# Optimization experiments

Measured on AMD Instinct MI355X. Metric: run time of the kernel, lower is better.

The kernel has to match this reference:

```python
import jax, jax.numpy as jnp
import numpy as np
import math

NUM_HEADS = 12
HEAD_DIM = 64
DEGREE = 3
POLY_DIM = HEAD_DIM * (DEGREE + 1)  # 256
MEM_HID = 512
HIDDEN = 768


def setup_inputs() -> dict:
    key = jax.random.key(0)
    ks = jax.random.split(key, 6)
    B, S = 4, 2048
    hidden_states = jax.random.normal(ks[0], (B, S, HIDDEN), dtype=jnp.float32)
    # q projection weight stored (in, out) so y = x @ Wq
    Wq = jax.random.normal(ks[1], (HIDDEN, HIDDEN), dtype=jnp.float32) / np.sqrt(HIDDEN)
    # polynomial coefficients initialized to 1/i!
    coeffs = jnp.array([1.0 / math.factorial(i) for i in range(DEGREE + 1)], dtype=jnp.float32)
    # deep memory MLP: Linear(poly_dim->mem_hid) + ReLU + Linear(mem_hid->poly_dim)
    W1 = jax.random.normal(ks[2], (POLY_DIM, MEM_HID), dtype=jnp.float32) / np.sqrt(POLY_DIM)
    b1 = jnp.zeros((MEM_HID,), dtype=jnp.float32)
    W2 = jax.random.normal(ks[3], (MEM_HID, POLY_DIM), dtype=jnp.float32) / np.sqrt(MEM_HID)
    b2 = jnp.zeros((POLY_DIM,), dtype=jnp.float32)
    return {"hidden_states": hidden_states, "Wq": Wq, "coeffs": coeffs,
            "W1": W1, "b1": b1, "W2": W2, "b2": b2}


def _poly_map(x, coeffs):
    # x: [..., head_dim] -> [..., head_dim*(degree+1)]
    xs = jnp.clip(x, -10.0, 10.0)
    feats = [coeffs[0] * jnp.ones_like(x)]
    for i in range(1, DEGREE + 1):
        feats.append(jnp.clip(coeffs[i] * xs ** i, -1e6, 1e6))
    return jnp.concatenate(feats, axis=-1)


def reference(hidden_states, Wq, coeffs, W1, b1, W2, b2):
    B, S, H = hidden_states.shape
    # q projection -> [B, S, nh, hd]
    q = (hidden_states @ Wq).reshape(B, S, NUM_HEADS, HEAD_DIM)
    # polynomial feature expansion -> [B, S, nh, poly_dim]
    poly_q = _poly_map(q, coeffs)
    flat = poly_q.reshape(-1, POLY_DIM)  # [B*S*nh, poly_dim]
    # deep memory MLP (test-time memory read)
    h = jax.nn.relu(flat @ W1 + b1)
    mem = h @ W2 + b2  # [B*S*nh, poly_dim]
    # slice first head_dim dims, fold heads back into hidden
    out = mem[:, :HEAD_DIM].reshape(B, S, NUM_HEADS * HEAD_DIM)
    return out
```

## Files before the change

kernel.cpp:

```cpp
#include <hip/hip_runtime.h>


typedef unsigned short u16;
typedef __attribute__((ext_vector_type(8))) short short8;
typedef __attribute__((ext_vector_type(4))) float f32x4;
typedef __attribute__((ext_vector_type(4))) u16 u16x4;

__device__ __forceinline__ u16 f2bf(float f) {
    unsigned u = __builtin_bit_cast(unsigned, f);
    u += 0x7FFFu + ((u >> 16) & 1u);
    return (u16)(u >> 16);
}

__device__ __forceinline__ unsigned cvtpk_bf16(float lo, float hi) {
    unsigned r;
    asm("v_cvt_pk_bf16_f32 %0, %1, %2" : "=v"(r) : "v"(lo), "v"(hi));
    return r;
}

__device__ __forceinline__ void gl2lds16(const void* g, void* l) {
    __builtin_amdgcn_global_load_lds(
        (const __attribute__((address_space(1))) unsigned int*)g,
        (__attribute__((address_space(3))) unsigned int*)l, 16, 0, 0);
}

#define WAIT_VM_LGKM_BAR(N) \
    asm volatile("s_waitcnt vmcnt(" #N ") lgkmcnt(0)\n\ts_barrier" ::: "memory")
#define WAIT_LGKM_BAR() \
    asm volatile("s_waitcnt lgkmcnt(0)\n\ts_barrier" ::: "memory")


__global__ __launch_bounds__(256)
void prep(const float* __restrict__ X, u16* __restrict__ Xb,
          const float* __restrict__ Wq, u16* __restrict__ Wqb,
          const float* __restrict__ W1, u16* __restrict__ W1b,
          const float* __restrict__ W2, u16* __restrict__ W2b,
          const float* __restrict__ b1, const float* __restrict__ coeffs,
          float* __restrict__ b1e)
{
    __shared__ float t[32][33];
    const int b = blockIdx.x, tid = threadIdx.x;

    if (b < 6144) {
        const int i = b * 256 + tid;
        float4 v = reinterpret_cast<const float4*>(X)[i];
        u16x4 o = {f2bf(v.x), f2bf(v.y), f2bf(v.z), f2bf(v.w)};
        reinterpret_cast<u16x4*>(Xb)[i] = o;
    } else if (b < 6880) {
        const float* in; u16* out; int R, Cin, bx, by;
        int lb = b - 6144;
        if (lb < 576)      { in = Wq; out = Wqb; R = 768; Cin = 768; bx = lb % 24; by = lb / 24; }
        else if (lb < 704) { lb -= 576; in = W1; out = W1b; R = 256; Cin = 512; bx = lb % 16; by = lb / 16; }
        else               { lb -= 704; in = W2; out = W2b; R = 512; Cin = 256; bx = lb % 2;  by = lb / 2; }
        const int c0 = bx * 32, r0 = by * 32;
        const int tx = tid & 31, ty = tid >> 5;
        #pragma unroll
        for (int j = 0; j < 32; j += 8)
            t[ty + j][tx] = in[(size_t)(r0 + ty + j) * Cin + c0 + tx];
        __syncthreads();
        #pragma unroll
        for (int j = 0; j < 32; j += 8)
            out[(size_t)(c0 + ty + j) * R + r0 + tx] = f2bf(t[tx][ty + j]);
    } else {
        const int n = (b - 6880) * 256 + tid;
        float s = 0.f;
        #pragma unroll 8
        for (int k = 0; k < 64; ++k) s += W1[k * 512 + n];
        b1e[n] = b1[n] + coeffs[0] * s;
    }
}


__global__ __launch_bounds__(256, 3)
void gemm1_poly(const u16* __restrict__ Xb, const u16* __restrict__ Wqb,
                const float* __restrict__ coeffs, u16* __restrict__ P)
{
    __shared__ u16 lds[128 * 200];

    const int tid = threadIdx.x;
    const int w = tid >> 6, lane = tid & 63;
    const int lrow = lane >> 2, lslot = lane & 3;
    const int m16 = lane & 15, quad = lane >> 4;
    const int w0 = w & 1, w1 = w >> 1;
    const int tok0 = blockIdx.x * 64;
    const int bn = blockIdx.y * 128;
    const int h0 = blockIdx.y * 2;

    const float c1 = coeffs[1], c2 = coeffs[2], c3 = coeffs[3];

    f32x4 acc[4][2];
    #pragma unroll
    for (int i = 0; i < 4; ++i)
        #pragma unroll
        for (int j = 0; j < 2; ++j)
            acc[i][j] = (f32x4){0.f, 0.f, 0.f, 0.f};

    auto stage = [&](int slot, int g) {
        const int k0 = g * 32;
        u16* Xs = lds + slot * 6144;
        u16* Ws = Xs + 2048;
        {
            const int row = w * 16 + lrow;
            const int cc = lslot ^ ((row >> 2) & 3);
            gl2lds16(Xb + (size_t)(tok0 + row) * 768 + k0 + cc * 8, &Xs[row * 32 + lslot * 8]);
        }
        #pragma unroll
        for (int i = 0; i < 2; ++i) {
            const int row = (w * 2 + i) * 16 + lrow;
            const int cc = lslot ^ ((row >> 2) & 3);
            gl2lds16(Wqb + (size_t)(bn + row) * 768 + k0 + cc * 8, &Ws[row * 32 + lslot * 8]);
        }
    };

    stage(0, 0);
    stage(1, 1);

    #pragma unroll 1
    for (int g = 0; g < 24; ++g) {
        WAIT_VM_LGKM_BAR(3);
        const int gg = (g + 2 <= 23) ? g + 2 : 23;
        stage((g + 2) % 3, gg);
        const u16* Xs = lds + (g % 3) * 6144;
        const u16* Ws = Xs + 2048;
        short8 a[4], b[2];
        #pragma unroll
        for (int i = 0; i < 4; ++i) {
            const int row = w0 * 64 + i * 16 + m16;
            const int ss = quad ^ ((row >> 2) & 3);
            a[i] = *reinterpret_cast<const short8*>(&Ws[row * 32 + ss * 8]);
        }
        #pragma unroll
        for (int j = 0; j < 2; ++j) {
            const int row = w1 * 32 + j * 16 + m16;
            const int ss = quad ^ ((row >> 2) & 3);
            b[j] = *reinterpret_cast<const short8*>(&Xs[row * 32 + ss * 8]);
        }
        #pragma unroll
        for (int i = 0; i < 4; ++i)
            #pragma unroll
            for (int j = 0; j < 2; ++j)
                acc[i][j] = __builtin_amdgcn_mfma_f32_16x16x32_bf16(a[i], b[j], acc[i][j], 0, 0, 0);
    }

    asm volatile("s_waitcnt vmcnt(0) lgkmcnt(0)\n\ts_barrier" ::: "memory");

    #pragma unroll
    for (int i = 0; i < 4; ++i) {
        const int d0 = i * 16 + quad * 4;
        #pragma unroll
        for (int j = 0; j < 2; ++j) {
            const int tokLocal = w1 * 32 + j * 16 + m16;
            u16* base = &lds[(tokLocal * 2 + w0) * 200 + d0];
            float x[4], x2[4];
            #pragma unroll
            for (int r = 0; r < 4; ++r) {
                x[r] = fminf(fmaxf(acc[i][j][r], -10.f), 10.f);
                x2[r] = x[r] * x[r];
            }
            uint2 p1, p2, p3;
            p1.x = cvtpk_bf16(c1 * x[0], c1 * x[1]);
            p1.y = cvtpk_bf16(c1 * x[2], c1 * x[3]);
            p2.x = cvtpk_bf16(c2 * x2[0], c2 * x2[1]);
            p2.y = cvtpk_bf16(c2 * x2[2], c2 * x2[3]);
            p3.x = cvtpk_bf16(c3 * x2[0] * x[0], c3 * x2[1] * x[1]);
            p3.y = cvtpk_bf16(c3 * x2[2] * x[2], c3 * x2[3] * x[3]);
            *reinterpret_cast<uint2*>(base)       = p1;
            *reinterpret_cast<uint2*>(base + 64)  = p2;
            *reinterpret_cast<uint2*>(base + 128) = p3;
        }
    }
    __syncthreads();

    #pragma unroll
    for (int ii = 0; ii < 12; ++ii) {
        const int flat = ii * 256 + tid;
        const int rowL = flat / 24, ck = flat % 24;
        const int tokL = rowL >> 1, hh = rowL & 1;
        const size_t prow = ((size_t)(tok0 + tokL) * 12 + h0 + hh);
        short8 v = *reinterpret_cast<const short8*>(&lds[rowL * 200 + ck * 8]);
        *reinterpret_cast<short8*>(P + prow * 192 + ck * 8) = v;
    }
}


__global__ __launch_bounds__(256, 2)
void gemm23(const u16* __restrict__ P, const u16* __restrict__ W1t,
            const float* __restrict__ b1e, const u16* __restrict__ W2t,
            const float* __restrict__ b2, float* __restrict__ out)
{
    __shared__ u16 ring[3][8192];
    __shared__ u16 Hs[4][128 * 32];

    const int tid = threadIdx.x;
    const int w = tid >> 6, lane = tid & 63;
    const int lrow = lane >> 2, lslot = lane & 3;
    const int m16 = lane & 15, quad = lane >> 4;
    const size_t r0 = (size_t)blockIdx.x * 128;
    const int w0 = w & 1, w1 = w >> 1;

    auto stageTo = [&](int slot, int g) {
        const int s = g / 6, c = g % 6;
        u16* W1s = ring[slot];
        u16* Ps  = ring[slot] + 4096;
        #pragma unroll
        for (int i = 0; i < 2; ++i) {
            const int row = (w * 2 + i) * 16 + lrow;
            const int cc = lslot ^ ((row >> 2) & 3);
            gl2lds16(W1t + (size_t)(s * 128 + row) * 256 + 64 + c * 32 + cc * 8,
                     &W1s[row * 32 + lslot * 8]);
            gl2lds16(P + (r0 + row) * 192 + c * 32 + cc * 8,
                     &Ps[row * 32 + lslot * 8]);
        }
    };
    auto stageClamped = [&](int slot, int gg) {
        if (gg <= 23) stageTo(slot, gg);
        else if (gg == 24) stageTo(slot, 23);
    };

    short8 b3s[4][2];
    auto loadW2 = [&](int s) {
        #pragma unroll
        for (int c = 0; c < 4; ++c)
            #pragma unroll
            for (int j = 0; j < 2; ++j)
                b3s[c][j] = *reinterpret_cast<const short8*>(
                    W2t + (size_t)(w1 * 32 + j * 16 + m16) * 512 + s * 128 + c * 32 + quad * 8);
    };

    f32x4 accO[4][2];
    #pragma unroll
    for (int i = 0; i < 4; ++i)
        #pragma unroll
        for (int j = 0; j < 2; ++j)
            accO[i][j] = (f32x4){0.f, 0.f, 0.f, 0.f};

    stageTo(0, 0);
    stageTo(1, 1);

    #pragma unroll 1
    for (int s = 0; s < 4; ++s) {
        f32x4 accH[4][4];
        #pragma unroll
        for (int i = 0; i < 4; ++i)
            #pragma unroll
            for (int j = 0; j < 4; ++j)
                accH[i][j] = (f32x4){0.f, 0.f, 0.f, 0.f};

        auto computeH = [&](int slot) {
            const u16* W1s = ring[slot];
            const u16* Ps  = ring[slot] + 4096;
            short8 af[4], bf[4];
            #pragma unroll
            for (int i = 0; i < 4; ++i) {
                const int row = w0 * 64 + i * 16 + m16;
                const int ss = quad ^ ((row >> 2) & 3);
                af[i] = *reinterpret_cast<const short8*>(&W1s[row * 32 + ss * 8]);
            }
            #pragma unroll
            for (int j = 0; j < 4; ++j) {
                const int row = w1 * 64 + j * 16 + m16;
                const int ss = quad ^ ((row >> 2) & 3);
                bf[j] = *reinterpret_cast<const short8*>(&Ps[row * 32 + ss * 8]);
            }
            #pragma unroll
            for (int i = 0; i < 4; ++i)
                #pragma unroll
                for (int j = 0; j < 4; ++j)
                    accH[i][j] = __builtin_amdgcn_mfma_f32_16x16x32_bf16(af[i], bf[j], accH[i][j], 0, 0, 0);
        };

        const int g0 = s * 6;
        WAIT_VM_LGKM_BAR(4);  stageClamped(2, g0 + 2); loadW2(s); computeH(0);
        WAIT_VM_LGKM_BAR(12); stageClamped(0, g0 + 3);            computeH(1);
        WAIT_VM_LGKM_BAR(4);  stageClamped(1, g0 + 4);            computeH(2);
        WAIT_VM_LGKM_BAR(4);  stageClamped(2, g0 + 5);            computeH(0);
        WAIT_VM_LGKM_BAR(4);  stageClamped(0, g0 + 6);            computeH(1);
        WAIT_VM_LGKM_BAR(4);  stageClamped(1, g0 + 7);            computeH(2);

        #pragma unroll
        for (int i = 0; i < 4; ++i) {
            const int lb = w0 * 64 + i * 16 + quad * 4;
            const f32x4 bv = *reinterpret_cast<const f32x4*>(&b1e[s * 128 + lb]);
            const int hc = lb >> 5;
            #pragma unroll
            for (int j = 0; j < 4; ++j) {
                const int tc = w1 * 64 + j * 16 + m16;
                const float h0 = fmaxf(accH[i][j][0] + bv[0], 0.f);
                const float h1 = fmaxf(accH[i][j][1] + bv[1], 0.f);
                const float h2 = fmaxf(accH[i][j][2] + bv[2], 0.f);
                const float h3 = fmaxf(accH[i][j][3] + bv[3], 0.f);
                uint2 v;
                v.x = cvtpk_bf16(h0, h1);
                v.y = cvtpk_bf16(h2, h3);
                const int sl = ((lb >> 3) & 3) ^ ((tc >> 2) & 3);
                *reinterpret_cast<uint2*>(&Hs[hc][tc * 32 + sl * 8 + (lb & 7)]) = v;
            }
        }

        WAIT_LGKM_BAR();

        #pragma unroll
        for (int c = 0; c < 4; ++c) {
            short8 a3[4];
            #pragma unroll
            for (int i = 0; i < 4; ++i) {
                const int tr = w0 * 64 + i * 16 + m16;
                const int ss = quad ^ ((tr >> 2) & 3);
                a3[i] = *reinterpret_cast<const short8*>(&Hs[c][tr * 32 + ss * 8]);
            }
            #pragma unroll
            for (int i = 0; i < 4; ++i)
                #pragma unroll
                for (int j = 0; j < 2; ++j)
                    accO[i][j] = __builtin_amdgcn_mfma_f32_16x16x32_bf16(a3[i], b3s[c][j], accO[i][j], 0, 0, 0);
        }
    }

    asm volatile("s_waitcnt vmcnt(0)" ::: "memory");

    #pragma unroll
    for (int j = 0; j < 2; ++j) {
        const int col = w1 * 32 + j * 16 + m16;
        const float bv = b2[col];
        #pragma unroll
        for (int i = 0; i < 4; ++i) {
            #pragma unroll
            for (int r = 0; r < 4; ++r) {
                const int row = w0 * 64 + i * 16 + quad * 4 + r;
                out[(r0 + row) * 64 + col] = accO[i][j][r] + bv;
            }
        }
    }
}


extern "C" void kernel_launch(void* const* d_in, const int* in_sizes, int n_in,
                              void* d_out, int out_size, void* d_ws, size_t ws_size,
                              hipStream_t stream) {
    const float* X      = (const float*)d_in[0];
    const float* Wq     = (const float*)d_in[1];
    const float* coeffs = (const float*)d_in[2];
    const float* W1     = (const float*)d_in[3];
    const float* b1     = (const float*)d_in[4];
    const float* W2     = (const float*)d_in[5];
    const float* b2     = (const float*)d_in[6];

    char* ws = (char*)d_ws;
    u16*   Xb  = (u16*)(ws);
    u16*   Wqb = (u16*)(ws + 12582912);
    u16*   W1b = (u16*)(ws + 13762560);
    u16*   W2b = (u16*)(ws + 14024704);
    float* b1e = (float*)(ws + 14090240);
    u16*   P   = (u16*)(ws + 14092288);

    prep<<<6882, 256, 0, stream>>>(X, Xb, Wq, Wqb, W1, W1b, W2, W2b, b1, coeffs, b1e);

    gemm1_poly<<<dim3(128, 6), 256, 0, stream>>>(Xb, Wqb, coeffs, P);

    gemm23<<<dim3(768), 256, 0, stream>>>(P, W1b, b1e, W2b, b2, (float*)d_out);
}
```

Before: 166.2 us.

## Fuse q-projection, polynomial expansion and memory MLP into one kernel

After: 151.0 us. -9.1%, faster.

```diff
diff --git a/kernel.cpp b/kernel.cpp
--- a/kernel.cpp
+++ b/kernel.cpp
@@ -28,7 +28,6 @@
     asm volatile("s_waitcnt vmcnt(" #N ") lgkmcnt(0)\n\ts_barrier" ::: "memory")
 #define WAIT_LGKM_BAR() \
     asm volatile("s_waitcnt lgkmcnt(0)\n\ts_barrier" ::: "memory")
-
 
 __global__ __launch_bounds__(256)
 void prep(const float* __restrict__ X, u16* __restrict__ Xb,
@@ -71,11 +70,14 @@
 }
 
 
-__global__ __launch_bounds__(256, 3)
-void gemm1_poly(const u16* __restrict__ Xb, const u16* __restrict__ Wqb,
-                const float* __restrict__ coeffs, u16* __restrict__ P)
+__global__ __launch_bounds__(256, 2)
+void fused(const u16* __restrict__ Xb, const u16* __restrict__ Wqb,
+           const float* __restrict__ coeffs,
+           const u16* __restrict__ W1t, const float* __restrict__ b1e,
+           const u16* __restrict__ W2t, const float* __restrict__ b2,
+           float* __restrict__ out)
 {
-    __shared__ u16 lds[128 * 200];
+    __shared__ u16 shm[37888];
 
     const int tid = threadIdx.x;
     const int w = tid >> 6, lane = tid & 63;
@@ -88,6 +90,11 @@
 
     const float c1 = coeffs[1], c2 = coeffs[2], c3 = coeffs[3];
 
+    u16* const qt    = shm;
+    u16* const ring1 = shm + 9216;
+    u16* const ring2 = shm + 9216;
+    u16* const HsB   = shm + 21504;
+
     f32x4 acc[4][2];
     #pragma unroll
     for (int i = 0; i < 4; ++i)
@@ -95,9 +102,9 @@
         for (int j = 0; j < 2; ++j)
             acc[i][j] = (f32x4){0.f, 0.f, 0.f, 0.f};
 
-    auto stage = [&](int slot, int g) {
+    auto stage1 = [&](int slot, int g) {
         const int k0 = g * 32;
-        u16* Xs = lds + slot * 6144;
+        u16* Xs = ring1 + slot * 6144;
         u16* Ws = Xs + 2048;
         {
             const int row = w * 16 + lrow;
@@ -112,15 +119,14 @@
         }
     };
 
-    stage(0, 0);
-    stage(1, 1);
+    stage1(0, 0);
+    stage1(1, 1);
 
     #pragma unroll 1
     for (int g = 0; g < 24; ++g) {
         WAIT_VM_LGKM_BAR(3);
-        const int gg = (g + 2 <= 23) ? g + 2 : 23;
-        stage((g + 2) % 3, gg);
-        const u16* Xs = lds + (g % 3) * 6144;
+        stage1((g + 2) % 3, (g + 2 <= 23) ? g + 2 : 23);
+        const u16* Xs = ring1 + (g % 3) * 6144;
         const u16* Ws = Xs + 2048;
         short8 a[4], b[2];
         #pragma unroll
@@ -135,11 +141,13 @@
             const int ss = quad ^ ((row >> 2) & 3);
             b[j] = *reinterpret_cast<const short8*>(&Xs[row * 32 + ss * 8]);
         }
+        __builtin_amdgcn_s_setprio(1);
         #pragma unroll
         for (int i = 0; i < 4; ++i)
             #pragma unroll
             for (int j = 0; j < 2; ++j)
                 acc[i][j] = __builtin_amdgcn_mfma_f32_16x16x32_bf16(a[i], b[j], acc[i][j], 0, 0, 0);
+        __builtin_amdgcn_s_setprio(0);
     }
 
     asm volatile("s_waitcnt vmcnt(0) lgkmcnt(0)\n\ts_barrier" ::: "memory");
@@ -149,72 +157,32 @@
         const int d0 = i * 16 + quad * 4;
         #pragma unroll
         for (int j = 0; j < 2; ++j) {
-            const int tokLocal = w1 * 32 + j * 16 + m16;
-            u16* base = &lds[(tokLocal * 2 + w0) * 200 + d0];
-            float x[4], x2[4];
-            #pragma unroll
-            for (int r = 0; r < 4; ++r) {
-                x[r] = fminf(fmaxf(acc[i][j][r], -10.f), 10.f);
-                x2[r] = x[r] * x[r];
-            }
-            uint2 p1, p2, p3;
-            p1.x = cvtpk_bf16(c1 * x[0], c1 * x[1]);
-            p1.y = cvtpk_bf16(c1 * x[2], c1 * x[3]);
-            p2.x = cvtpk_bf16(c2 * x2[0], c2 * x2[1]);
-            p2.y = cvtpk_bf16(c2 * x2[2], c2 * x2[3]);
-            p3.x = cvtpk_bf16(c3 * x2[0] * x[0], c3 * x2[1] * x[1]);
-            p3.y = cvtpk_bf16(c3 * x2[2] * x[2], c3 * x2[3] * x[3]);
-            *reinterpret_cast<uint2*>(base)       = p1;
-            *reinterpret_cast<uint2*>(base + 64)  = p2;
-            *reinterpret_cast<uint2*>(base + 128) = p3;
-        }
-    }
-    __syncthreads();
-
-    #pragma unroll
-    for (int ii = 0; ii < 12; ++ii) {
-        const int flat = ii * 256 + tid;
-        const int rowL = flat / 24, ck = flat % 24;
-        const int tokL = rowL >> 1, hh = rowL & 1;
-        const size_t prow = ((size_t)(tok0 + tokL) * 12 + h0 + hh);
-        short8 v = *reinterpret_cast<const short8*>(&lds[rowL * 200 + ck * 8]);
-        *reinterpret_cast<short8*>(P + prow * 192 + ck * 8) = v;
-    }
-}
-
-
-__global__ __launch_bounds__(256, 2)
-void gemm23(const u16* __restrict__ P, const u16* __restrict__ W1t,
-            const float* __restrict__ b1e, const u16* __restrict__ W2t,
-            const float* __restrict__ b2, float* __restrict__ out)
-{
-    __shared__ u16 ring[3][8192];
-    __shared__ u16 Hs[4][128 * 32];
-
-    const int tid = threadIdx.x;
-    const int w = tid >> 6, lane = tid & 63;
-    const int lrow = lane >> 2, lslot = lane & 3;
-    const int m16 = lane & 15, quad = lane >> 4;
-    const size_t r0 = (size_t)blockIdx.x * 128;
-    const int w0 = w & 1, w1 = w >> 1;
-
-    auto stageTo = [&](int slot, int g) {
+            const int l = (w1 * 32 + j * 16 + m16) * 2 + w0;
+            float x0 = fminf(fmaxf(acc[i][j][0], -10.f), 10.f);
+            float x1 = fminf(fmaxf(acc[i][j][1], -10.f), 10.f);
+            float x2 = fminf(fmaxf(acc[i][j][2], -10.f), 10.f);
+            float x3 = fminf(fmaxf(acc[i][j][3], -10.f), 10.f);
+            uint2 v;
+            v.x = cvtpk_bf16(x0, x1);
+            v.y = cvtpk_bf16(x2, x3);
+            *reinterpret_cast<uint2*>(&qt[l * 72 + d0]) = v;
+        }
+    }
+
+    auto stage2 = [&](int slot, int g) {
         const int s = g / 6, c = g % 6;
-        u16* W1s = ring[slot];
-        u16* Ps  = ring[slot] + 4096;
+        u16* W1s = ring2 + slot * 4096;
         #pragma unroll
         for (int i = 0; i < 2; ++i) {
             const int row = (w * 2 + i) * 16 + lrow;
             const int cc = lslot ^ ((row >> 2) & 3);
             gl2lds16(W1t + (size_t)(s * 128 + row) * 256 + 64 + c * 32 + cc * 8,
                      &W1s[row * 32 + lslot * 8]);
-            gl2lds16(P + (r0 + row) * 192 + c * 32 + cc * 8,
-                     &Ps[row * 32 + lslot * 8]);
         }
     };
-    auto stageClamped = [&](int slot, int gg) {
-        if (gg <= 23) stageTo(slot, gg);
-        else if (gg == 24) stageTo(slot, 23);
+    auto stage2c = [&](int slot, int gg) {
+        if (gg <= 23) stage2(slot, gg);
+        else if (gg == 24) stage2(slot, 23);
     };
 
     short8 b3s[4][2];
@@ -234,8 +202,8 @@
         for (int j = 0; j < 2; ++j)
             accO[i][j] = (f32x4){0.f, 0.f, 0.f, 0.f};
 
-    stageTo(0, 0);
-    stageTo(1, 1);
+    stage2(0, 0);
+    stage2(1, 1);
 
     #pragma unroll 1
     for (int s = 0; s < 4; ++s) {
@@ -246,9 +214,8 @@
             for (int j = 0; j < 4; ++j)
                 accH[i][j] = (f32x4){0.f, 0.f, 0.f, 0.f};
 
-        auto computeH = [&](int slot) {
-            const u16* W1s = ring[slot];
-            const u16* Ps  = ring[slot] + 4096;
+        auto computeH = [&](int slot, int c) {
+            const u16* W1s = ring2 + slot * 4096;
             short8 af[4], bf[4];
             #pragma unroll
             for (int i = 0; i < 4; ++i) {
@@ -259,23 +226,39 @@
             #pragma unroll
             for (int j = 0; j < 4; ++j) {
                 const int row = w1 * 64 + j * 16 + m16;
-                const int ss = quad ^ ((row >> 2) & 3);
-                bf[j] = *reinterpret_cast<const short8*>(&Ps[row * 32 + ss * 8]);
-            }
+                short8 qv = *reinterpret_cast<const short8*>(
+                    &qt[row * 72 + (c & 1) * 32 + quad * 8]);
+                float y[8];
+                #pragma unroll
+                for (int e = 0; e < 8; ++e) {
+                    float x = __builtin_bit_cast(float, ((unsigned)(u16)qv[e]) << 16);
+                    if (c < 2)      y[e] = c1 * x;
+                    else if (c < 4) y[e] = c2 * (x * x);
+                    else            y[e] = (c3 * (x * x)) * x;
+                }
+                uint4 pk;
+                pk.x = cvtpk_bf16(y[0], y[1]);
+                pk.y = cvtpk_bf16(y[2], y[3]);
+                pk.z = cvtpk_bf16(y[4], y[5]);
+                pk.w = cvtpk_bf16(y[6], y[7]);
+                bf[j] = __builtin_bit_cast(short8, pk);
+            }
+            __builtin_amdgcn_s_setprio(1);
             #pragma unroll
             for (int i = 0; i < 4; ++i)
                 #pragma unroll
                 for (int j = 0; j < 4; ++j)
                     accH[i][j] = __builtin_amdgcn_mfma_f32_16x16x32_bf16(af[i], bf[j], accH[i][j], 0, 0, 0);
+            __builtin_amdgcn_s_setprio(0);
         };
 
         const int g0 = s * 6;
-        WAIT_VM_LGKM_BAR(4);  stageClamped(2, g0 + 2); loadW2(s); computeH(0);
-        WAIT_VM_LGKM_BAR(12); stageClamped(0, g0 + 3);            computeH(1);
-        WAIT_VM_LGKM_BAR(4);  stageClamped(1, g0 + 4);            computeH(2);
-        WAIT_VM_LGKM_BAR(4);  stageClamped(2, g0 + 5);            computeH(0);
-        WAIT_VM_LGKM_BAR(4);  stageClamped(0, g0 + 6);            computeH(1);
-        WAIT_VM_LGKM_BAR(4);  stageClamped(1, g0 + 7);            computeH(2);
+        WAIT_VM_LGKM_BAR(2);  stage2c(2, g0 + 2); loadW2(s); computeH(0, 0);
+        WAIT_VM_LGKM_BAR(10); stage2c(0, g0 + 3);            computeH(1, 1);
+        WAIT_VM_LGKM_BAR(10); stage2c(1, g0 + 4);            computeH(2, 2);
+        WAIT_VM_LGKM_BAR(2);  stage2c(2, g0 + 5);            computeH(0, 3);
+        WAIT_VM_LGKM_BAR(2);  stage2c(0, g0 + 6);            computeH(1, 4);
+        WAIT_VM_LGKM_BAR(2);  stage2c(1, g0 + 7);            computeH(2, 5);
 
         #pragma unroll
         for (int i = 0; i < 4; ++i) {
@@ -285,20 +268,21 @@
             #pragma unroll
             for (int j = 0; j < 4; ++j) {
                 const int tc = w1 * 64 + j * 16 + m16;
-                const float h0 = fmaxf(accH[i][j][0] + bv[0], 0.f);
-                const float h1 = fmaxf(accH[i][j][1] + bv[1], 0.f);
-                const float h2 = fmaxf(accH[i][j][2] + bv[2], 0.f);
-                const float h3 = fmaxf(accH[i][j][3] + bv[3], 0.f);
+                const float h0v = fmaxf(accH[i][j][0] + bv[0], 0.f);
+                const float h1v = fmaxf(accH[i][j][1] + bv[1], 0.f);
+                const float h2v = fmaxf(accH[i][j][2] + bv[2], 0.f);
+                const float h3v = fmaxf(accH[i][j][3] + bv[3], 0.f);
                 uint2 v;
-                v.x = cvtpk_bf16(h0, h1);
-                v.y = cvtpk_bf16(h2, h3);
+                v.x = cvtpk_bf16(h0v, h1v);
+                v.y = cvtpk_bf16(h2v, h3v);
                 const int sl = ((lb >> 3) & 3) ^ ((tc >> 2) & 3);
-                *reinterpret_cast<uint2*>(&Hs[hc][tc * 32 + sl * 8 + (lb & 7)]) = v;
+                *reinterpret_cast<uint2*>(&HsB[hc * 4096 + tc * 32 + sl * 8 + (lb & 7)]) = v;
             }
         }
 
         WAIT_LGKM_BAR();
 
+        __builtin_amdgcn_s_setprio(1);
         #pragma unroll
         for (int c = 0; c < 4; ++c) {
             short8 a3[4];
@@ -306,7 +290,7 @@
             for (int i = 0; i < 4; ++i) {
                 const int tr = w0 * 64 + i * 16 + m16;
                 const int ss = quad ^ ((tr >> 2) & 3);
-                a3[i] = *reinterpret_cast<const short8*>(&Hs[c][tr * 32 + ss * 8]);
+                a3[i] = *reinterpret_cast<const short8*>(&HsB[c * 4096 + tr * 32 + ss * 8]);
             }
             #pragma unroll
             for (int i = 0; i < 4; ++i)
@@ -314,6 +298,7 @@
                 for (int j = 0; j < 2; ++j)
                     accO[i][j] = __builtin_amdgcn_mfma_f32_16x16x32_bf16(a3[i], b3s[c][j], accO[i][j], 0, 0, 0);
         }
+        __builtin_amdgcn_s_setprio(0);
     }
 
     asm volatile("s_waitcnt vmcnt(0)" ::: "memory");
@@ -326,8 +311,9 @@
         for (int i = 0; i < 4; ++i) {
             #pragma unroll
             for (int r = 0; r < 4; ++r) {
-                const int row = w0 * 64 + i * 16 + quad * 4 + r;
-                out[(r0 + row) * 64 + col] = accO[i][j][r] + bv;
+                const int l = w0 * 64 + i * 16 + quad * 4 + r;
+                const size_t orow = (size_t)(tok0 + (l >> 1)) * 12 + h0 + (l & 1);
+                out[orow * 64 + col] = accO[i][j][r] + bv;
             }
         }
     }
@@ -351,11 +337,9 @@
     u16*   W1b = (u16*)(ws + 13762560);
     u16*   W2b = (u16*)(ws + 14024704);
     float* b1e = (float*)(ws + 14090240);
-    u16*   P   = (u16*)(ws + 14092288);
 
     prep<<<6882, 256, 0, stream>>>(X, Xb, Wq, Wqb, W1, W1b, W2, W2b, b1, coeffs, b1e);
 
-    gemm1_poly<<<dim3(128, 6), 256, 0, stream>>>(Xb, Wqb, coeffs, P);
-
-    gemm23<<<dim3(768), 256, 0, stream>>>(P, W1b, b1e, W2b, b2, (float*)d_out);
-}
+    fused<<<dim3(128, 6), 256, 0, stream>>>(Xb, Wqb, coeffs, W1b, b1e, W2b, b2,
+                                            (float*)d_out);
+}
```
